# Performance work log

Hardware: AMD Instinct MI355X
Metric: run time of the kernel (lower is better)

The kernel has to match this reference:

```python
import jax, jax.numpy as jnp
import numpy as np

B, S, H = 2, 2048, 1024
NH, HD = 16, 64  # num heads, head dim
EPS = 1e-12

def layernorm(x, g, b):
    mu = jnp.mean(x, axis=-1, keepdims=True)
    var = jnp.mean(jnp.square(x - mu), axis=-1, keepdims=True)
    return (x - mu) / jnp.sqrt(var + EPS) * g + b

def setup_inputs() -> dict:
    key = jax.random.key(0)
    ks = jax.random.split(key, 6)
    sd = 0.02
    return {
        "x": jax.random.normal(ks[0], (B, S, H), jnp.float32),
        "ln1_g": jnp.ones((H,), jnp.float32),
        "ln1_b": jnp.zeros((H,), jnp.float32),
        "w_qkv": jax.random.normal(ks[1], (H, 3 * H), jnp.float32) * sd,
        "b_qkv": jnp.zeros((3 * H,), jnp.float32),
        "w_dense": jax.random.normal(ks[2], (H, H), jnp.float32) * sd,
        "b_dense": jnp.zeros((H,), jnp.float32),
        "ln2_g": jnp.ones((H,), jnp.float32),
        "ln2_b": jnp.zeros((H,), jnp.float32),
        "w_fc1": jax.random.normal(ks[3], (H, 2 * H), jnp.float32) * sd,
        "w_fc2": jax.random.normal(ks[4], (2 * H, H), jnp.float32) * sd,
        "b_fc2": jnp.zeros((H,), jnp.float32),
    }

def reference(x, ln1_g, ln1_b, w_qkv, b_qkv, w_dense, b_dense,
              ln2_g, ln2_b, w_fc1, w_fc2, b_fc2):
    b, s, h = x.shape
    qkv = layernorm(x, ln1_g, ln1_b) @ w_qkv + b_qkv          # (b, s, 3h)
    q, k, v = jnp.split(qkv, 3, axis=-1)
    # (b, s, h) -> (b, nh, s, hd)
    reshape = lambda t: t.reshape(b, s, NH, HD).transpose(0, 2, 1, 3)
    q, k, v = reshape(q), reshape(k), reshape(v)
    scores = jnp.einsum('bhqd,bhkd->bhqk', q, k) / jnp.sqrt(jnp.float32(HD))
    causal = jnp.tril(jnp.ones((s, s), dtype=bool))
    scores = jnp.where(causal, scores, -jnp.inf)
    probs = jax.nn.softmax(scores, axis=-1)
    attn = jnp.einsum('bhqk,bhkd->bhqd', probs, v)            # (b, nh, s, hd)
    attn = attn.transpose(0, 2, 1, 3).reshape(b, s, h)
    out = x + (attn @ w_dense + b_dense)
    m = layernorm(out, ln2_g, ln2_b)
    mlp = jax.nn.gelu(m @ w_fc1, approximate=False) @ w_fc2 + b_fc2
    return out + mlp
```

## Files before the change

kernel.cpp:

```cpp
#include <hip/hip_runtime.h>
#include <hip/hip_bf16.h>

typedef __bf16 bf16x8 __attribute__((ext_vector_type(8)));
typedef float  f32x4  __attribute__((ext_vector_type(4)));

typedef __attribute__((address_space(3))) unsigned int as3_u32;
typedef __attribute__((address_space(1))) unsigned int as1_u32;

__device__ __forceinline__ void gld_lds16(const void* gptr, void* lptr){
  __builtin_amdgcn_global_load_lds((const as1_u32*)gptr, (as3_u32*)lptr, 16, 0, 0);
}

__global__ __launch_bounds__(256) void transpose_all(
    const float* __restrict__ w_qkv, const float* __restrict__ w_dense,
    const float* __restrict__ w_fc1, const float* __restrict__ w_fc2,
    __bf16* __restrict__ oqkv, __bf16* __restrict__ oden,
    __bf16* __restrict__ ofc1, __bf16* __restrict__ ofc2){
  __shared__ float tile[32][33];
  int idx = blockIdx.x;
  const float* in; __bf16* out; int R, C;
  if (idx < 3072){ in = w_qkv;  out = oqkv; R = 1024; C = 3072; }
  else if (idx < 4096){ idx -= 3072; in = w_dense; out = oden; R = 1024; C = 1024; }
  else if (idx < 6144){ idx -= 4096; in = w_fc1;  out = ofc1; R = 1024; C = 2048; }
  else { idx -= 6144; in = w_fc2;  out = ofc2; R = 2048; C = 1024; }
  const int ntx = C >> 5;
  const int c0 = (idx % ntx)*32, r0 = (idx / ntx)*32;
  const int tx = threadIdx.x, ty = threadIdx.y;
  #pragma unroll
  for (int i=0;i<32;i+=8)
    tile[ty+i][tx] = in[(size_t)(r0+ty+i)*C + c0+tx];
  __syncthreads();
  #pragma unroll
  for (int i=0;i<32;i+=8)
    out[(size_t)(c0+ty+i)*R + r0+tx] = (__bf16)tile[tx][ty+i];
}

__global__ __launch_bounds__(256) void ln_kernel(const float* __restrict__ x, const float* __restrict__ g,
                                                 const float* __restrict__ b, __bf16* __restrict__ out){
  const int row = blockIdx.x, t = threadIdx.x;
  const float4 v = ((const float4*)(x + (size_t)row*1024))[t];
  float s = v.x+v.y+v.z+v.w;
  #pragma unroll
  for (int m=1;m<64;m<<=1) s += __shfl_xor(s, m);
  __shared__ float red[8];
  if ((t&63)==0) red[t>>6] = s;
  __syncthreads();
  const float mu = (red[0]+red[1]+red[2]+red[3]) * (1.f/1024.f);
  const float d0=v.x-mu, d1=v.y-mu, d2=v.z-mu, d3=v.w-mu;
  float sq = d0*d0+d1*d1+d2*d2+d3*d3;
  #pragma unroll
  for (int m=1;m<64;m<<=1) sq += __shfl_xor(sq, m);
  if ((t&63)==0) red[4+(t>>6)] = sq;
  __syncthreads();
  const float var = (red[4]+red[5]+red[6]+red[7]) * (1.f/1024.f);
  const float inv = rsqrtf(var + 1e-12f);
  const float4 gv = ((const float4*)g)[t];
  const float4 bv = ((const float4*)b)[t];
  union { __bf16 h[4]; uint2 u; } pk;
  pk.h[0]=(__bf16)(d0*inv*gv.x+bv.x); pk.h[1]=(__bf16)(d1*inv*gv.y+bv.y);
  pk.h[2]=(__bf16)(d2*inv*gv.z+bv.z); pk.h[3]=(__bf16)(d3*inv*gv.w+bv.w);
  *(uint2*)(out + (size_t)row*1024 + t*4) = pk.u;
}

template<int MODE>
__global__ __launch_bounds__(256) void gemm_bt(
    const __bf16* __restrict__ A, const __bf16* __restrict__ Bt,
    const float* __restrict__ bias,
    __bf16* __restrict__ outB,
    __bf16* __restrict__ qO, __bf16* __restrict__ kO, __bf16* __restrict__ vtO,
    int M, int N, int K)
{
  __shared__ __align__(16) __bf16 As[2][128*32];
  __shared__ __align__(16) __bf16 Bs[2][128*32];
  const int tid = threadIdx.x;
  const int lane = tid & 63, wave = tid >> 6;
  const int wr = wave >> 1, wc = wave & 1;
  const int l15 = lane & 15, lg = lane >> 4;
  const int bm = blockIdx.x, bn = blockIdx.y;
  const __bf16* Ab = A  + (size_t)bm*128*K;
  const __bf16* Bb = Bt + (size_t)bn*128*K;
  f32x4 acc[4][4] = {};
  const int r0 = tid >> 2;
  const int c0 = (tid & 3) * 8;

  auto stage = [&](int kt, int b){
    const int k0 = kt*32;
    char* dA = (char*)&As[b][0] + wave*1024;
    char* dB = (char*)&Bs[b][0] + wave*1024;
    gld_lds16(Ab + (size_t)r0*K      + k0 + c0, dA);
    gld_lds16(Ab + (size_t)(r0+64)*K + k0 + c0, dA + 4096);
    gld_lds16(Bb + (size_t)r0*K      + k0 + c0, dB);
    gld_lds16(Bb + (size_t)(r0+64)*K + k0 + c0, dB + 4096);
  };

  const int nk = K >> 5;
  stage(0, 0);
  __syncthreads();
  for (int kt = 0; kt < nk; ++kt){
    const int b = kt & 1;
    if (kt+1 < nk) stage(kt+1, b^1);
    bf16x8 af[4], bfv[4];
    #pragma unroll
    for (int i=0;i<4;++i){
      af[i]  = *(const bf16x8*)&As[b][(wr*64 + i*16 + l15)*32 + lg*8];
      bfv[i] = *(const bf16x8*)&Bs[b][(wc*64 + i*16 + l15)*32 + lg*8];
    }
    #pragma unroll
    for (int i=0;i<4;++i)
      #pragma unroll
      for (int j=0;j<4;++j)
        acc[i][j] = __builtin_amdgcn_mfma_f32_16x16x32_bf16(af[i], bfv[j], acc[i][j], 0,0,0);
    __syncthreads();
  }
  #pragma unroll
  for (int i=0;i<4;++i){
    #pragma unroll
    for (int j=0;j<4;++j){
      const int col = bn*128 + wc*64 + j*16 + l15;
      float bv;
      if constexpr (MODE==2) bv = 0.f; else bv = bias[col];
      #pragma unroll
      for (int r=0;r<4;++r){
        const int row = bm*128 + wr*64 + i*16 + lg*4 + r;
        float v = acc[i][j][r] + bv;
        if constexpr (MODE==0){
          const int b_ = row >> 11, s_ = row & 2047;
          if (col < 1024){
            const int h = col>>6, d = col&63;
            qO[((size_t)(b_*16+h)*2048 + s_)*64 + d] = (__bf16)v;
          } else if (col < 2048){
            const int h = (col-1024)>>6, d = (col-1024)&63;
            kO[((size_t)(b_*16+h)*2048 + s_)*64 + d] = (__bf16)v;
          } else {
            const int h = (col-2048)>>6, d = (col-2048)&63;
            vtO[((size_t)(b_*16+h)*64 + d)*2048 + s_] = (__bf16)v;
          }
        } else {
          const float gl = 0.5f*v*(1.f + erff(v*0.70710678118f));
          outB[(size_t)row*N + col] = (__bf16)gl;
        }
      }
    }
  }
}

__global__ __launch_bounds__(256) void gemm_bt64(
    const __bf16* __restrict__ A, const __bf16* __restrict__ Bt,
    const float* __restrict__ bias, const float* __restrict__ resid,
    float* __restrict__ outF, int M, int N, int K)
{
  __shared__ __align__(16) __bf16 As[2][128*32];
  __shared__ __align__(16) __bf16 Bs[2][64*32];
  const int tid = threadIdx.x;
  const int lane = tid & 63, wave = tid >> 6;
  const int l15 = lane & 15, lg = lane >> 4;
  const int bm = blockIdx.x, bn = blockIdx.y;
  const __bf16* Ab = A  + (size_t)bm*128*K;
  const __bf16* Bb = Bt + (size_t)bn*64*K;
  f32x4 acc[2][4] = {};
  const int r0 = tid >> 2;
  const int c0 = (tid & 3) * 8;

  auto stage = [&](int kt, int b){
    const int k0 = kt*32;
    char* dA = (char*)&As[b][0] + wave*1024;
    char* dB = (char*)&Bs[b][0] + wave*1024;
    gld_lds16(Ab + (size_t)r0*K      + k0 + c0, dA);
    gld_lds16(Ab + (size_t)(r0+64)*K + k0 + c0, dA + 4096);
    gld_lds16(Bb + (size_t)r0*K      + k0 + c0, dB);
  };

  const int nk = K >> 5;
  stage(0, 0);
  __syncthreads();
  for (int kt = 0; kt < nk; ++kt){
    const int b = kt & 1;
    if (kt+1 < nk) stage(kt+1, b^1);
    bf16x8 af[2], bfv[4];
    #pragma unroll
    for (int i=0;i<2;++i)
      af[i]  = *(const bf16x8*)&As[b][(wave*32 + i*16 + l15)*32 + lg*8];
    #pragma unroll
    for (int j=0;j<4;++j)
      bfv[j] = *(const bf16x8*)&Bs[b][(j*16 + l15)*32 + lg*8];
    #pragma unroll
    for (int i=0;i<2;++i)
      #pragma unroll
      for (int j=0;j<4;++j)
        acc[i][j] = __builtin_amdgcn_mfma_f32_16x16x32_bf16(af[i], bfv[j], acc[i][j], 0,0,0);
    __syncthreads();
  }
  #pragma unroll
  for (int i=0;i<2;++i){
    #pragma unroll
    for (int j=0;j<4;++j){
      const int col = bn*64 + j*16 + l15;
      const float bv = bias[col];
      #pragma unroll
      for (int r=0;r<4;++r){
        const int row = bm*128 + wave*32 + i*16 + lg*4 + r;
        outF[(size_t)row*N + col] = acc[i][j][r] + bv + resid[(size_t)row*N + col];
      }
    }
  }
}

__global__ __launch_bounds__(512, 4) void attn_kernel(
    const __bf16* __restrict__ Q, const __bf16* __restrict__ K,
    const __bf16* __restrict__ Vt, __bf16* __restrict__ out)
{
  __shared__ __align__(16) __bf16 Ks[2][128*64];
  __shared__ __align__(16) __bf16 Vs[2][2][64*64];
  __shared__ __align__(16) __bf16 Pl[8][16*64];
  const int tid = threadIdx.x;
  const int lane = tid & 63, wave = tid >> 6;
  const int l15 = lane & 15, lg = lane >> 4;
  const int bh = blockIdx.y;
  const int nqb = (int)gridDim.x;
  const int qblk = (bh & 16) ? (int)blockIdx.x : (nqb - 1 - (int)blockIdx.x);
  const int qb = qblk * 128;
  const int qw = qb + wave*16;
  const __bf16* Qh = Q + (size_t)bh*2048*64;
  const char*  Khc = (const char*)(K  + (size_t)bh*2048*64);
  const char*  Vhc = (const char*)(Vt + (size_t)bh*64*2048);

  bf16x8 qf[2];
  #pragma unroll
  for (int f=0;f<2;++f){
    bf16x8 t8 = *(const bf16x8*)&Qh[(size_t)(qw + l15)*64 + f*32 + lg*8];
    #pragma unroll
    for (int j=0;j<8;++j) t8[j] = (__bf16)((float)t8[j] * 0.125f);
    qf[f] = t8;
  }

  f32x4 oacc[4] = {};
  float mrun = -1e30f, lrun = 0.f;

  const int swz_st = (((lane&7) ^ (lane>>3)) << 4);
  const int rswz = ((l15 & 7) << 4);
  char* Pw = (char*)&Pl[wave][0];

  const int krow = wave*16 + (lane>>3);
  const int kh   = wave & 1;
  const int dgrp = wave >> 1;
  const int vrow = dgrp*16 + (lane>>3);

  const int nst = qblk + 1;

  {
    gld_lds16(Khc + (size_t)krow*128 + swz_st,     (char*)&Ks[0][0] + wave*2048);
    gld_lds16(Khc + (size_t)(krow+8)*128 + swz_st, (char*)&Ks[0][0] + wave*2048 + 1024);
    const char* s = Vhc + kh*128 + swz_st;
    gld_lds16(s + (size_t)vrow*4096,     (char*)&Vs[0][kh][0] + dgrp*2048);
    gld_lds16(s + (size_t)(vrow+8)*4096, (char*)&Vs[0][kh][0] + dgrp*2048 + 1024);
  }
  __syncthreads();

  for (int st = 0; st < nst; ++st){
    const int cur = st & 1;
    const int kv0 = st*128;
    if (st+1 < nst){
      const size_t nkv0 = (size_t)(kv0 + 128);
      gld_lds16(Khc + (nkv0 + krow)*128 + swz_st,     (char*)&Ks[cur^1][0] + wave*2048);
      gld_lds16(Khc + (nkv0 + krow + 8)*128 + swz_st, (char*)&Ks[cur^1][0] + wave*2048 + 1024);
      const char* s = Vhc + nkv0*2 + kh*128 + swz_st;
      gld_lds16(s + (size_t)vrow*4096,     (char*)&Vs[cur^1][kh][0] + dgrp*2048);
      gld_lds16(s + (size_t)(vrow+8)*4096, (char*)&Vs[cur^1][kh][0] + dgrp*2048 + 1024);
    }
    if (kv0 <= qw + 15){
      const char* Kb = (const char*)&Ks[cur][0];
      f32x4 sc[8];
      #pragma unroll
      for (int t=0;t<8;++t) sc[t] = f32x4{0.f,0.f,0.f,0.f};
      #pragma unroll
      for (int t=0;t<8;++t){
        const int row = t*16 + l15;
        bf16x8 k0 = *(const bf16x8*)(Kb + row*128 + ((lg*16)      ^ rswz));
        bf16x8 k1 = *(const bf16x8*)(Kb + row*128 + ((64 + lg*16) ^ rswz));
        sc[t] = __builtin_amdgcn_mfma_f32_16x16x32_bf16(k0, qf[0], sc[t], 0,0,0);
        sc[t] = __builtin_amdgcn_mfma_f32_16x16x32_bf16(k1, qf[1], sc[t], 0,0,0);
      }
      if (kv0 + 127 > qw){
        const int q = qw + l15;
        #pragma unroll
        for (int t=0;t<8;++t)
          #pragma unroll
          for (int r=0;r<4;++r)
            if (kv0 + t*16 + lg*4 + r > q) sc[t][r] = -1e30f;
      }
      f32x4 mm;
      #pragma unroll
      for (int r=0;r<4;++r){
        float a = fmaxf(fmaxf(sc[0][r],sc[1][r]), fmaxf(sc[2][r],sc[3][r]));
        float b = fmaxf(fmaxf(sc[4][r],sc[5][r]), fmaxf(sc[6][r],sc[7][r]));
        mm[r] = fmaxf(a,b);
      }
      float mx = fmaxf(fmaxf(mm[0],mm[1]), fmaxf(mm[2],mm[3]));
      mx = fmaxf(mx, __shfl_xor(mx, 16));
      mx = fmaxf(mx, __shfl_xor(mx, 32));
      if (!__all(mx <= mrun + 8.0f)){
        const float nm = fmaxf(mrun, mx);
        const float co = exp2f((mrun - nm) * 1.44269504f);
        lrun *= co;
        float cor[4];
        #pragma unroll
        for (int r=0;r<4;++r) cor[r] = __shfl(co, lg*4+r);
        #pragma unroll
        for (int c=0;c<4;++c)
          #pragma unroll
          for (int r=0;r<4;++r)
            oacc[c][r] *= cor[r];
        mrun = nm;
      }
      const float mb = mrun * 1.44269504f;
      #pragma unroll
      for (int t=0;t<8;++t)
        #pragma unroll
        for (int r=0;r<4;++r)
          sc[t][r] = exp2f(sc[t][r]*1.44269504f - mb);
      f32x4 ss;
      #pragma unroll
      for (int r=0;r<4;++r){
        float a = (sc[0][r]+sc[1][r]) + (sc[2][r]+sc[3][r]);
        float b = (sc[4][r]+sc[5][r]) + (sc[6][r]+sc[7][r]);
        ss[r] = a + b;
      }
      float rs = (ss[0]+ss[1]) + (ss[2]+ss[3]);
      rs += __shfl_xor(rs, 16);
      rs += __shfl_xor(rs, 32);
      lrun += rs;
      #pragma unroll
      for (int h=0; h<2; ++h){
        #pragma unroll
        for (int t=0;t<4;++t){
          union { __bf16 hh[4]; uint2 u; } pk4;
          pk4.hh[0] = (__bf16)sc[h*4+t][0];
          pk4.hh[1] = (__bf16)sc[h*4+t][1];
          pk4.hh[2] = (__bf16)sc[h*4+t][2];
          pk4.hh[3] = (__bf16)sc[h*4+t][3];
          *(uint2*)(Pw + l15*128 + ((t*32 + lg*8) ^ rswz)) = pk4.u;
        }
        const char* Vb = (const char*)&Vs[cur][h][0];
        #pragma unroll
        for (int f=0;f<2;++f){
          bf16x8 pa = *(const bf16x8*)(Pw + l15*128 + ((f*64 + lg*16) ^ rswz));
          #pragma unroll
          for (int c=0;c<4;++c){
            bf16x8 vf = *(const bf16x8*)(Vb + (c*16+l15)*128 + ((f*64 + lg*16) ^ rswz));
            oacc[c] = __builtin_amdgcn_mfma_f32_16x16x32_bf16(pa, vf, oacc[c], 0,0,0);
          }
        }
      }
    }
    __syncthreads();
  }

  const int b_ = bh >> 4, h_ = bh & 15;
  float lr[4];
  #pragma unroll
  for (int r=0;r<4;++r) lr[r] = __shfl(lrun, lg*4+r);
  #pragma unroll
  for (int c=0;c<4;++c)
    #pragma unroll
    for (int r=0;r<4;++r){
      const int row = qw + lg*4 + r;
      out[((size_t)(b_*2048 + row))*1024 + h_*64 + c*16 + l15] = (__bf16)(oacc[c][r] / lr[r]);
    }
}

extern "C" void kernel_launch(void* const* d_in, const int* in_sizes, int n_in,
                              void* d_out, int out_size, void* d_ws, size_t ws_size,
                              hipStream_t stream) {
  const float* x      = (const float*)d_in[0];
  const float* ln1_g  = (const float*)d_in[1];
  const float* ln1_b  = (const float*)d_in[2];
  const float* w_qkv  = (const float*)d_in[3];
  const float* b_qkv  = (const float*)d_in[4];
  const float* w_dense= (const float*)d_in[5];
  const float* b_dense= (const float*)d_in[6];
  const float* ln2_g  = (const float*)d_in[7];
  const float* ln2_b  = (const float*)d_in[8];
  const float* w_fc1  = (const float*)d_in[9];
  const float* w_fc2  = (const float*)d_in[10];
  const float* b_fc2  = (const float*)d_in[11];

  char* ws = (char*)d_ws;
  __bf16* wqkvT  = (__bf16*)(ws + 0);
  __bf16* wdenT  = (__bf16*)(ws + 6291456);
  __bf16* wfc1T  = (__bf16*)(ws + 8388608);
  __bf16* wfc2T  = (__bf16*)(ws + 12582912);
  __bf16* xn     = (__bf16*)(ws + 16777216);
  __bf16* Qb     = (__bf16*)(ws + 25165824);
  __bf16* Kb     = (__bf16*)(ws + 33554432);
  __bf16* Vtb    = (__bf16*)(ws + 41943040);
  __bf16* attnb  = (__bf16*)(ws + 50331648);
  float*  outf   = (float*) (ws + 58720256);
  __bf16* mb     = (__bf16*)(ws + 75497472);
  __bf16* h1b    = (__bf16*)(ws + 83886080);

  transpose_all<<<8192, dim3(32,8), 0, stream>>>(w_qkv, w_dense, w_fc1, w_fc2,
                                                 wqkvT, wdenT, wfc1T, wfc2T);
  ln_kernel<<<4096, 256, 0, stream>>>(x, ln1_g, ln1_b, xn);
  gemm_bt<0><<<dim3(32,24), 256, 0, stream>>>(xn, wqkvT, b_qkv,
                                              nullptr, Qb, Kb, Vtb, 4096, 3072, 1024);
  attn_kernel<<<dim3(16,32), 512, 0, stream>>>(Qb, Kb, Vtb, attnb);
  gemm_bt64<<<dim3(32,16), 256, 0, stream>>>(attnb, wdenT, b_dense, x,
                                             outf, 4096, 1024, 1024);
  ln_kernel<<<4096, 256, 0, stream>>>(outf, ln2_g, ln2_b, mb);
  gemm_bt<2><<<dim3(32,16), 256, 0, stream>>>(mb, wfc1T, nullptr,
                                              h1b, nullptr, nullptr, nullptr, 4096, 2048, 1024);
  gemm_bt64<<<dim3(32,16), 256, 0, stream>>>(h1b, wfc2T, b_fc2, outf,
                                             (float*)d_out, 4096, 1024, 2048);
}
```

Before: 192.4 us.

## Use 8-wave GEMM blocks with swizzled LDS, setprio, and causal QK skip

Both GEMM kernels move from 256 to 512 threads per block, with each wave computing a smaller sub-tile. The aim is more waves per CU and more latency hiding. The LDS layout gets an XOR swizzle on staging and fragment reads to cut bank conflicts. s_setprio is wrapped around the MFMA sections in the GEMMs and in attention, and the attention QK^T skips 16-row key tiles lying wholly above the causal diagonal. In exchange, each wave reuses fewer operands per MFMA, and more blocks compete for LDS.

```diff
diff --git a/kernel.cpp b/kernel.cpp
--- a/kernel.cpp
+++ b/kernel.cpp
@@ -63,7 +63,7 @@
 }
 
 template<int MODE>
-__global__ __launch_bounds__(256) void gemm_bt(
+__global__ __launch_bounds__(512, 6) void gemm_bt(
     const __bf16* __restrict__ A, const __bf16* __restrict__ Bt,
     const float* __restrict__ bias,
     __bf16* __restrict__ outB,
@@ -74,23 +74,20 @@
   __shared__ __align__(16) __bf16 Bs[2][128*32];
   const int tid = threadIdx.x;
   const int lane = tid & 63, wave = tid >> 6;
-  const int wr = wave >> 1, wc = wave & 1;
+  const int wm = wave >> 2, wn = wave & 3;
   const int l15 = lane & 15, lg = lane >> 4;
   const int bm = blockIdx.x, bn = blockIdx.y;
   const __bf16* Ab = A  + (size_t)bm*128*K;
   const __bf16* Bb = Bt + (size_t)bn*128*K;
-  f32x4 acc[4][4] = {};
-  const int r0 = tid >> 2;
-  const int c0 = (tid & 3) * 8;
+  f32x4 acc[4][2] = {};
+  const int r0  = tid >> 2;
+  const int c0s = ((tid & 3) * 8) ^ (((r0 >> 1) & 3) << 3);
+  const int fswz = ((l15 >> 1) & 3) << 4;
 
   auto stage = [&](int kt, int b){
     const int k0 = kt*32;
-    char* dA = (char*)&As[b][0] + wave*1024;
-    char* dB = (char*)&Bs[b][0] + wave*1024;
-    gld_lds16(Ab + (size_t)r0*K      + k0 + c0, dA);
-    gld_lds16(Ab + (size_t)(r0+64)*K + k0 + c0, dA + 4096);
-    gld_lds16(Bb + (size_t)r0*K      + k0 + c0, dB);
-    gld_lds16(Bb + (size_t)(r0+64)*K + k0 + c0, dB + 4096);
+    gld_lds16(Ab + (size_t)r0*K + k0 + c0s, (char*)&As[b][0] + wave*1024);
+    gld_lds16(Bb + (size_t)r0*K + k0 + c0s, (char*)&Bs[b][0] + wave*1024);
   };
 
   const int nk = K >> 5;
@@ -99,29 +96,32 @@
   for (int kt = 0; kt < nk; ++kt){
     const int b = kt & 1;
     if (kt+1 < nk) stage(kt+1, b^1);
-    bf16x8 af[4], bfv[4];
-    #pragma unroll
-    for (int i=0;i<4;++i){
-      af[i]  = *(const bf16x8*)&As[b][(wr*64 + i*16 + l15)*32 + lg*8];
-      bfv[i] = *(const bf16x8*)&Bs[b][(wc*64 + i*16 + l15)*32 + lg*8];
-    }
+    bf16x8 af[4], bfv[2];
     #pragma unroll
     for (int i=0;i<4;++i)
-      #pragma unroll
-      for (int j=0;j<4;++j)
+      af[i]  = *(const bf16x8*)((const char*)&As[b][0] + (wm*64 + i*16 + l15)*64 + ((lg*16) ^ fswz));
+    #pragma unroll
+    for (int j=0;j<2;++j)
+      bfv[j] = *(const bf16x8*)((const char*)&Bs[b][0] + (wn*32 + j*16 + l15)*64 + ((lg*16) ^ fswz));
+    __builtin_amdgcn_s_setprio(1);
+    #pragma unroll
+    for (int i=0;i<4;++i)
+      #pragma unroll
+      for (int j=0;j<2;++j)
         acc[i][j] = __builtin_amdgcn_mfma_f32_16x16x32_bf16(af[i], bfv[j], acc[i][j], 0,0,0);
+    __builtin_amdgcn_s_setprio(0);
     __syncthreads();
   }
   #pragma unroll
   for (int i=0;i<4;++i){
     #pragma unroll
-    for (int j=0;j<4;++j){
-      const int col = bn*128 + wc*64 + j*16 + l15;
+    for (int j=0;j<2;++j){
+      const int col = bn*128 + wn*32 + j*16 + l15;
       float bv;
       if constexpr (MODE==2) bv = 0.f; else bv = bias[col];
       #pragma unroll
       for (int r=0;r<4;++r){
-        const int row = bm*128 + wr*64 + i*16 + lg*4 + r;
+        const int row = bm*128 + wm*64 + i*16 + lg*4 + r;
         float v = acc[i][j][r] + bv;
         if constexpr (MODE==0){
           const int b_ = row >> 11, s_ = row & 2047;
@@ -144,7 +144,7 @@
   }
 }
 
-__global__ __launch_bounds__(256) void gemm_bt64(
+__global__ __launch_bounds__(512, 6) void gemm_bt64(
     const __bf16* __restrict__ A, const __bf16* __restrict__ Bt,
     const float* __restrict__ bias, const float* __restrict__ resid,
     float* __restrict__ outF, int M, int N, int K)
@@ -153,21 +153,21 @@
   __shared__ __align__(16) __bf16 Bs[2][64*32];
   const int tid = threadIdx.x;
   const int lane = tid & 63, wave = tid >> 6;
+  const int wm = wave >> 1, wn = wave & 1;
   const int l15 = lane & 15, lg = lane >> 4;
   const int bm = blockIdx.x, bn = blockIdx.y;
   const __bf16* Ab = A  + (size_t)bm*128*K;
   const __bf16* Bb = Bt + (size_t)bn*64*K;
-  f32x4 acc[2][4] = {};
-  const int r0 = tid >> 2;
-  const int c0 = (tid & 3) * 8;
+  f32x4 acc[2][2] = {};
+  const int r0  = tid >> 2;
+  const int c0s = ((tid & 3) * 8) ^ (((r0 >> 1) & 3) << 3);
+  const int fswz = ((l15 >> 1) & 3) << 4;
 
   auto stage = [&](int kt, int b){
     const int k0 = kt*32;
-    char* dA = (char*)&As[b][0] + wave*1024;
-    char* dB = (char*)&Bs[b][0] + wave*1024;
-    gld_lds16(Ab + (size_t)r0*K      + k0 + c0, dA);
-    gld_lds16(Ab + (size_t)(r0+64)*K + k0 + c0, dA + 4096);
-    gld_lds16(Bb + (size_t)r0*K      + k0 + c0, dB);
+    gld_lds16(Ab + (size_t)r0*K + k0 + c0s, (char*)&As[b][0] + wave*1024);
+    if (wave < 4)
+      gld_lds16(Bb + (size_t)r0*K + k0 + c0s, (char*)&Bs[b][0] + wave*1024);
   };
 
   const int nk = K >> 5;
@@ -176,29 +176,31 @@
   for (int kt = 0; kt < nk; ++kt){
     const int b = kt & 1;
     if (kt+1 < nk) stage(kt+1, b^1);
-    bf16x8 af[2], bfv[4];
+    bf16x8 af[2], bfv[2];
     #pragma unroll
     for (int i=0;i<2;++i)
-      af[i]  = *(const bf16x8*)&As[b][(wave*32 + i*16 + l15)*32 + lg*8];
-    #pragma unroll
-    for (int j=0;j<4;++j)
-      bfv[j] = *(const bf16x8*)&Bs[b][(j*16 + l15)*32 + lg*8];
+      af[i]  = *(const bf16x8*)((const char*)&As[b][0] + (wm*32 + i*16 + l15)*64 + ((lg*16) ^ fswz));
+    #pragma unroll
+    for (int j=0;j<2;++j)
+      bfv[j] = *(const bf16x8*)((const char*)&Bs[b][0] + (wn*32 + j*16 + l15)*64 + ((lg*16) ^ fswz));
+    __builtin_amdgcn_s_setprio(1);
     #pragma unroll
     for (int i=0;i<2;++i)
       #pragma unroll
-      for (int j=0;j<4;++j)
+      for (int j=0;j<2;++j)
         acc[i][j] = __builtin_amdgcn_mfma_f32_16x16x32_bf16(af[i], bfv[j], acc[i][j], 0,0,0);
+    __builtin_amdgcn_s_setprio(0);
     __syncthreads();
   }
   #pragma unroll
   for (int i=0;i<2;++i){
     #pragma unroll
-    for (int j=0;j<4;++j){
-      const int col = bn*64 + j*16 + l15;
+    for (int j=0;j<2;++j){
+      const int col = bn*64 + wn*32 + j*16 + l15;
       const float bv = bias[col];
       #pragma unroll
       for (int r=0;r<4;++r){
-        const int row = bm*128 + wave*32 + i*16 + lg*4 + r;
+        const int row = bm*128 + wm*32 + i*16 + lg*4 + r;
         outF[(size_t)row*N + col] = acc[i][j][r] + bv + resid[(size_t)row*N + col];
       }
     }
@@ -272,14 +274,18 @@
       f32x4 sc[8];
       #pragma unroll
       for (int t=0;t<8;++t) sc[t] = f32x4{0.f,0.f,0.f,0.f};
+      __builtin_amdgcn_s_setprio(1);
       #pragma unroll
       for (int t=0;t<8;++t){
-        const int row = t*16 + l15;
-        bf16x8 k0 = *(const bf16x8*)(Kb + row*128 + ((lg*16)      ^ rswz));
-        bf16x8 k1 = *(const bf16x8*)(Kb + row*128 + ((64 + lg*16) ^ rswz));
-        sc[t] = __builtin_amdgcn_mfma_f32_16x16x32_bf16(k0, qf[0], sc[t], 0,0,0);
-        sc[t] = __builtin_amdgcn_mfma_f32_16x16x32_bf16(k1, qf[1], sc[t], 0,0,0);
-      }
+        if (kv0 + t*16 <= qw + 15){
+          const int row = t*16 + l15;
+          bf16x8 k0 = *(const bf16x8*)(Kb + row*128 + ((lg*16)      ^ rswz));
+          bf16x8 k1 = *(const bf16x8*)(Kb + row*128 + ((64 + lg*16) ^ rswz));
+          sc[t] = __builtin_amdgcn_mfma_f32_16x16x32_bf16(k0, qf[0], sc[t], 0,0,0);
+          sc[t] = __builtin_amdgcn_mfma_f32_16x16x32_bf16(k1, qf[1], sc[t], 0,0,0);
+        }
+      }
+      __builtin_amdgcn_s_setprio(0);
       if (kv0 + 127 > qw){
         const int q = qw + l15;
         #pragma unroll
@@ -341,6 +347,7 @@
           *(uint2*)(Pw + l15*128 + ((t*32 + lg*8) ^ rswz)) = pk4.u;
         }
         const char* Vb = (const char*)&Vs[cur][h][0];
+        __builtin_amdgcn_s_setprio(1);
         #pragma unroll
         for (int f=0;f<2;++f){
           bf16x8 pa = *(const bf16x8*)(Pw + l15*128 + ((f*64 + lg*16) ^ rswz));
@@ -350,6 +357,7 @@
             oacc[c] = __builtin_amdgcn_mfma_f32_16x16x32_bf16(pa, vf, oacc[c], 0,0,0);
           }
         }
+        __builtin_amdgcn_s_setprio(0);
       }
     }
     __syncthreads();
@@ -401,14 +409,14 @@
   transpose_all<<<8192, dim3(32,8), 0, stream>>>(w_qkv, w_dense, w_fc1, w_fc2,
                                                  wqkvT, wdenT, wfc1T, wfc2T);
   ln_kernel<<<4096, 256, 0, stream>>>(x, ln1_g, ln1_b, xn);
-  gemm_bt<0><<<dim3(32,24), 256, 0, stream>>>(xn, wqkvT, b_qkv,
+  gemm_bt<0><<<dim3(32,24), 512, 0, stream>>>(xn, wqkvT, b_qkv,
                                               nullptr, Qb, Kb, Vtb, 4096, 3072, 1024);
   attn_kernel<<<dim3(16,32), 512, 0, stream>>>(Qb, Kb, Vtb, attnb);
-  gemm_bt64<<<dim3(32,16), 256, 0, stream>>>(attnb, wdenT, b_dense, x,
+  gemm_bt64<<<dim3(32,16), 512, 0, stream>>>(attnb, wdenT, b_dense, x,
                                              outf, 4096, 1024, 1024);
   ln_kernel<<<4096, 256, 0, stream>>>(outf, ln2_g, ln2_b, mb);
-  gemm_bt<2><<<dim3(32,16), 256, 0, stream>>>(mb, wfc1T, nullptr,
+  gemm_bt<2><<<dim3(32,16), 512, 0, stream>>>(mb, wfc1T, nullptr,
                                               h1b, nullptr, nullptr, nullptr, 4096, 2048, 1024);
-  gemm_bt64<<<dim3(32,16), 256, 0, stream>>>(h1b, wfc2T, b_fc2, outf,
+  gemm_bt64<<<dim3(32,16), 512, 0, stream>>>(h1b, wfc2T, b_fc2, outf,
                                              (float*)d_out, 4096, 1024, 2048);
 }
```

New measurement: 394.4 us. +105.0%, slower.
